# Performance work log

Hardware: AMD Instinct MI355X
Metric: run time of the kernel (lower is better)

Reference implementation:

```python
import jax, jax.numpy as jnp
import numpy as np

MAX_BITS = 64
HIDDEN = 256
EPS = 1e-5
TEMPERATURE = 1.0  # buffer default


def _layernorm(x, gamma, beta):
    mu = jnp.mean(x, axis=-1, keepdims=True)
    var = jnp.var(x, axis=-1, keepdims=True)
    return (x - mu) * jax.lax.rsqrt(var + EPS) * gamma + beta


def setup_inputs() -> dict:
    key = jax.random.key(0)
    ks = jax.random.split(key, 8)
    B = 32768
    # binary-ish inputs in [0,1)
    a_bits = (jax.random.uniform(ks[0], (B, MAX_BITS)) < 0.5).astype(jnp.float32)
    shift_bits = (jax.random.uniform(ks[1], (B, MAX_BITS)) < 0.5).astype(jnp.float32)
    # decoder: Linear(64,256) -> LN -> ReLU -> Linear(256,256) -> LN -> ReLU -> Linear(256,64)
    def lin(k, out_d, in_d):
        bound = 1.0 / np.sqrt(in_d)
        kw, kb = jax.random.split(k)
        W = jax.random.uniform(kw, (out_d, in_d), minval=-bound, maxval=bound)
        b = jax.random.uniform(kb, (out_d,), minval=-bound, maxval=bound)
        return W, b
    W1, b1 = lin(ks[2], HIDDEN, MAX_BITS)
    W2, b2 = lin(ks[3], HIDDEN, HIDDEN)
    W3, b3 = lin(ks[4], MAX_BITS, HIDDEN)
    g1 = jnp.ones((HIDDEN,)); be1 = jnp.zeros((HIDDEN,))
    g2 = jnp.ones((HIDDEN,)); be2 = jnp.zeros((HIDDEN,))
    return {
        "a_bits": a_bits, "shift_bits": shift_bits,
        "W1": W1, "b1": b1, "g1": g1, "be1": be1,
        "W2": W2, "b2": b2, "g2": g2, "be2": be2,
        "W3": W3, "b3": b3,
    }


def reference(a_bits, shift_bits, W1, b1, g1, be1, W2, b2, g2, be2, W3, b3):
    bits = a_bits.shape[1]
    # 2-layer MLP decoder
    h = jax.nn.relu(_layernorm(shift_bits @ W1.T + b1, g1, be1))
    h = jax.nn.relu(_layernorm(h @ W2.T + b2, g2, be2))
    shift_logits = (h @ W3.T + b3)[:, :bits]
    # training path: softmax over shift positions
    shift_probs = jax.nn.softmax(shift_logits / TEMPERATURE, axis=-1)
    # Toeplitz shift-sum: out[b,i] = sum_{s<=i} probs[b,s] * a_bits[b,i-s]
    i = jnp.arange(bits)[:, None]
    s = jnp.arange(bits)[None, :]
    idx = i - s                       # [bits, bits]
    mask = (idx >= 0)
    gath = a_bits[:, jnp.where(mask, idx, 0)] * mask.astype(a_bits.dtype)  # [B, bits, bits]
    return jnp.einsum('bis,bs->bi', gath, shift_probs)
```

## Files before the change

kernel.cpp:

```cpp
#include <hip/hip_runtime.h>
#include <hip/hip_fp16.h>


typedef short s8v __attribute__((ext_vector_type(8)));
typedef float f4v __attribute__((ext_vector_type(4)));

#define HPAD 264
#define PPAD 68

#define OFF_W1F 0
#define OFF_W2F 16384
#define OFF_W3F 81920
#define OFF_B1  98304
#define OFF_G1  98560
#define OFF_BE1 98816
#define OFF_B2  99072
#define OFF_G2  99328
#define OFF_BE2 99584
#define OFF_B3  99840

__device__ __forceinline__ float b2f(unsigned short u) {
    union { unsigned int i; float f; } v; v.i = ((unsigned int)u) << 16; return v.f;
}
__device__ __forceinline__ unsigned short f2b(float f) {
    union { float f; unsigned int i; } v; v.f = f;
    return (unsigned short)((v.i + 0x7fffu + ((v.i >> 16) & 1u)) >> 16);
}
__device__ __forceinline__ unsigned int cvtpk(float a, float b) {
    unsigned int r;
    asm("v_cvt_pk_bf16_f32 %0, %1, %2" : "=v"(r) : "v"(a), "v"(b));
    return r;
}
__device__ __forceinline__ int h2i(__half2 h) { union { __half2 h; int i; } u; u.h = h; return u.i; }
__device__ __forceinline__ __half2 i2h(int i) { union { __half2 h; int i; } u; u.i = i; return u.h; }

__device__ __forceinline__ bool probe_bf16(const void* a_bits) {
    unsigned int wv = ((const unsigned int*)a_bits)[threadIdx.x & 63];
    return __ballot((wv & 0xffffu) == 0x3f80u) != 0ULL;
}

__global__ __launch_bounds__(256) void convert_kernel(
    const void* __restrict__ a_probe,
    const void* __restrict__ W1, const void* __restrict__ W2, const void* __restrict__ W3,
    const void* __restrict__ b1, const void* __restrict__ g1, const void* __restrict__ be1,
    const void* __restrict__ b2, const void* __restrict__ g2, const void* __restrict__ be2,
    const void* __restrict__ b3,
    unsigned short* __restrict__ ws)
{
    const bool isbf = probe_bf16(a_probe);
    const int t = blockIdx.x * 256 + threadIdx.x;

    if (t < 12288) {
        const void* W; int K, idx, dstbase;
        if (t < 2048)       { idx = t;         W = W1; K = 64;  dstbase = OFF_W1F + idx * 8; }
        else if (t < 10240) { idx = t - 2048;  W = W2; K = 256; dstbase = OFF_W2F + idx * 8; }
        else                { idx = t - 10240; W = W3; K = 256; dstbase = OFF_W3F + idx * 8; }
        int nt, kc, lane;
        if (t < 2048) { nt = idx >> 7; kc = (idx >> 6) & 1; lane = idx & 63; }
        else          { nt = idx >> 9; kc = (idx >> 6) & 7; lane = idx & 63; }
        const int row = nt * 16 + (lane & 15);
        const int col = kc * 32 + (lane >> 4) * 8;
        const int src = row * K + col;
        s8v o;
        if (isbf) {
            o = *(const s8v*)((const unsigned short*)W + src);
        } else {
            const float* f = (const float*)W + src;
#pragma unroll
            for (int j = 0; j < 8; ++j) o[j] = (short)f2b(f[j]);
        }
        *(s8v*)(ws + dstbase) = o;
    } else if (t < 12488) {
        const int v = t - 12288;
        const void* srcp; int base, off;
        if (v < 32)       { srcp = b1;  base = OFF_B1;  off = v * 8; }
        else if (v < 64)  { srcp = g1;  base = OFF_G1;  off = (v - 32) * 8; }
        else if (v < 96)  { srcp = be1; base = OFF_BE1; off = (v - 64) * 8; }
        else if (v < 128) { srcp = b2;  base = OFF_B2;  off = (v - 96) * 8; }
        else if (v < 160) { srcp = g2;  base = OFF_G2;  off = (v - 128) * 8; }
        else if (v < 192) { srcp = be2; base = OFF_BE2; off = (v - 160) * 8; }
        else              { srcp = b3;  base = OFF_B3;  off = (v - 192) * 8; }
#pragma unroll
        for (int j = 0; j < 8; ++j)
            ws[base + off + j] = isbf ? ((const unsigned short*)srcp)[off + j]
                                      : f2b(((const float*)srcp)[off + j]);
    }
}

template<bool BF16>
__device__ __forceinline__ float loadS(const void* p, int idx) {
    if constexpr (BF16) return b2f(((const unsigned short*)p)[idx]);
    else return ((const float*)p)[idx];
}
template<bool BF16>
__device__ __forceinline__ s8v loadA8(const void* p, int idx) {
    if constexpr (BF16) {
        return *(const s8v*)((const unsigned short*)p + idx);
    } else {
        const float* f = (const float*)p + idx;
        f4v a = *(const f4v*)f;
        f4v b = *(const f4v*)(f + 4);
        union { s8v s; unsigned int u[4]; } r;
        r.u[0] = cvtpk(a[0], a[1]);
        r.u[1] = cvtpk(a[2], a[3]);
        r.u[2] = cvtpk(b[0], b[1]);
        r.u[3] = cvtpk(b[2], b[3]);
        return r.s;
    }
}
template<bool BF16>
__device__ __forceinline__ void storeO(void* p, int idx, float v) {
    if constexpr (BF16) ((unsigned short*)p)[idx] = f2b(v);
    else ((float*)p)[idx] = v;
}

__device__ __forceinline__ void ln_relu_store(
    f4v* acc, const unsigned short* ws, int offB, int offG, int offBe,
    short* Hs, float* SS, int w, int q, int c, int row, int ntb)
{
    float sm[2][4], sv[2][4];
#pragma unroll
    for (int mt = 0; mt < 2; ++mt)
#pragma unroll
        for (int r = 0; r < 4; ++r) { sm[mt][r] = 0.f; sv[mt][r] = 0.f; }
#pragma unroll
    for (int i = 0; i < 4; ++i) {
        const float bias = b2f(ws[offB + (ntb + i) * 16 + c]);
#pragma unroll
        for (int mt = 0; mt < 2; ++mt)
#pragma unroll
            for (int r = 0; r < 4; ++r) {
                float v = acc[mt * 4 + i][r] + bias;
                acc[mt * 4 + i][r] = v;
                sm[mt][r] += v; sv[mt][r] += v * v;
            }
    }
#pragma unroll
    for (int m = 1; m <= 8; m <<= 1)
#pragma unroll
        for (int mt = 0; mt < 2; ++mt)
#pragma unroll
            for (int r = 0; r < 4; ++r) {
                sm[mt][r] += __shfl_xor(sm[mt][r], m, 64);
                sv[mt][r] += __shfl_xor(sv[mt][r], m, 64);
            }
    if (c == 0)
#pragma unroll
        for (int mt = 0; mt < 2; ++mt)
#pragma unroll
            for (int r = 0; r < 4; ++r) {
                const int g = mt * 16 + row + r;
                *(float2*)&SS[g * 8 + w * 2] = make_float2(sm[mt][r], sv[mt][r]);
            }
    __syncthreads();
#pragma unroll
    for (int mt = 0; mt < 2; ++mt)
#pragma unroll
        for (int r = 0; r < 4; ++r) {
            const int g = mt * 16 + row + r;
            f4v v0 = *(const f4v*)&SS[g * 8];
            f4v v1 = *(const f4v*)&SS[g * 8 + 4];
            float st = v0[0] + v0[2] + v1[0] + v1[2];
            float sq = v0[1] + v0[3] + v1[1] + v1[3];
            float mean = st * (1.0f / 256.0f);
            float var  = fmaxf(sq * (1.0f / 256.0f) - mean * mean, 0.0f);
            sm[mt][r] = mean; sv[mt][r] = rsqrtf(var + 1e-5f);
        }
#pragma unroll
    for (int i = 0; i < 4; ++i) {
        const int nt = ntb + i;
        const float gg = b2f(ws[offG + nt * 16 + c]);
        const float bb = b2f(ws[offBe + nt * 16 + c]);
#pragma unroll
        for (int mt = 0; mt < 2; ++mt) {
            float y[4];
#pragma unroll
            for (int r = 0; r < 4; ++r)
                y[r] = fmaxf((acc[mt * 4 + i][r] - sm[mt][r]) * sv[mt][r] * gg + bb, 0.0f);
            unsigned int u01 = cvtpk(y[0], y[1]);
            unsigned int u23 = cvtpk(y[2], y[3]);
            Hs[(mt * 16 + row + 0) * HPAD + nt * 16 + c] = (short)(u01 & 0xffffu);
            Hs[(mt * 16 + row + 1) * HPAD + nt * 16 + c] = (short)(u01 >> 16);
            Hs[(mt * 16 + row + 2) * HPAD + nt * 16 + c] = (short)(u23 & 0xffffu);
            Hs[(mt * 16 + row + 3) * HPAD + nt * 16 + c] = (short)(u23 >> 16);
        }
    }
}

template<bool BF16>
__device__ __forceinline__ void pipeline(
    const void* a_bits, const void* shifts, const unsigned short* ws, void* out,
    short* Hs, float* Ps, float* SS)
{
    const int tid = threadIdx.x;
    const int w = tid >> 6;
    const int l = tid & 63;
    const int q = l >> 4;
    const int c = l & 15;
    const int ntb = w << 2;
    const int grow0 = (int)blockIdx.x << 5;
    const int row = q * 4;

    f4v acc1[8];
#pragma unroll
    for (int i = 0; i < 8; ++i) acc1[i] = (f4v){0.f, 0.f, 0.f, 0.f};

    const s8v xa00 = loadA8<BF16>(shifts, (grow0 + c) * 64 + q * 8);
    const s8v xa01 = loadA8<BF16>(shifts, (grow0 + c) * 64 + 32 + q * 8);
    const s8v xa10 = loadA8<BF16>(shifts, (grow0 + 16 + c) * 64 + q * 8);
    const s8v xa11 = loadA8<BF16>(shifts, (grow0 + 16 + c) * 64 + 32 + q * 8);
#pragma unroll
    for (int i = 0; i < 4; ++i) {
        const int nt = ntb + i;
        s8v wb0 = *(const s8v*)(ws + OFF_W1F + ((nt * 2 + 0) * 64 + l) * 8);
        s8v wb1 = *(const s8v*)(ws + OFF_W1F + ((nt * 2 + 1) * 64 + l) * 8);
        acc1[i]     = __builtin_amdgcn_mfma_f32_16x16x32_bf16(xa00, wb0, acc1[i], 0, 0, 0);
        acc1[i]     = __builtin_amdgcn_mfma_f32_16x16x32_bf16(xa01, wb1, acc1[i], 0, 0, 0);
        acc1[4 + i] = __builtin_amdgcn_mfma_f32_16x16x32_bf16(xa10, wb0, acc1[4 + i], 0, 0, 0);
        acc1[4 + i] = __builtin_amdgcn_mfma_f32_16x16x32_bf16(xa11, wb1, acc1[4 + i], 0, 0, 0);
    }
    ln_relu_store(acc1, ws, OFF_B1, OFF_G1, OFF_BE1, Hs, SS, w, q, c, row, ntb);
    __syncthreads();

    f4v acc2[8];
#pragma unroll
    for (int i = 0; i < 8; ++i) acc2[i] = (f4v){0.f, 0.f, 0.f, 0.f};
#pragma unroll
    for (int ks = 0; ks < 8; ++ks) {
        s8v af0 = *(const s8v*)&Hs[c * HPAD + ks * 32 + q * 8];
        s8v af1 = *(const s8v*)&Hs[(16 + c) * HPAD + ks * 32 + q * 8];
#pragma unroll
        for (int i = 0; i < 4; ++i) {
            s8v bf_ = *(const s8v*)(ws + OFF_W2F + (((ntb + i) * 8 + ks) * 64 + l) * 8);
            acc2[i]     = __builtin_amdgcn_mfma_f32_16x16x32_bf16(af0, bf_, acc2[i], 0, 0, 0);
            acc2[4 + i] = __builtin_amdgcn_mfma_f32_16x16x32_bf16(af1, bf_, acc2[4 + i], 0, 0, 0);
        }
    }
    ln_relu_store(acc2, ws, OFF_B2, OFF_G2, OFF_BE2, Hs, SS, w, q, c, row, ntb);
    __syncthreads();

    f4v acc3[2];
#pragma unroll
    for (int t = 0; t < 2; ++t) acc3[t] = (f4v){0.f, 0.f, 0.f, 0.f};
#pragma unroll
    for (int ks = 0; ks < 8; ++ks) {
        s8v af0 = *(const s8v*)&Hs[c * HPAD + ks * 32 + q * 8];
        s8v af1 = *(const s8v*)&Hs[(16 + c) * HPAD + ks * 32 + q * 8];
        s8v bf_ = *(const s8v*)(ws + OFF_W3F + ((w * 8 + ks) * 64 + l) * 8);
        acc3[0] = __builtin_amdgcn_mfma_f32_16x16x32_bf16(af0, bf_, acc3[0], 0, 0, 0);
        acc3[1] = __builtin_amdgcn_mfma_f32_16x16x32_bf16(af1, bf_, acc3[1], 0, 0, 0);
    }
    {
        const float bias = b2f(ws[OFF_B3 + w * 16 + c]);
        float sum[2][4];
#pragma unroll
        for (int mt = 0; mt < 2; ++mt)
#pragma unroll
            for (int r = 0; r < 4; ++r) {
                float e = __expf(acc3[mt][r] + bias);
                Ps[(mt * 16 + row + r) * PPAD + w * 16 + c] = e;
                sum[mt][r] = e;
            }
#pragma unroll
        for (int m = 1; m <= 8; m <<= 1)
#pragma unroll
            for (int mt = 0; mt < 2; ++mt)
#pragma unroll
                for (int r = 0; r < 4; ++r)
                    sum[mt][r] += __shfl_xor(sum[mt][r], m, 64);
        if (c == 0)
#pragma unroll
            for (int mt = 0; mt < 2; ++mt)
#pragma unroll
                for (int r = 0; r < 4; ++r)
                    SS[(mt * 16 + row + r) * 8 + w * 2 + 1] = sum[mt][r];
    }
    __syncthreads();

#pragma unroll
    for (int jj = 0; jj < 4; ++jj) {
        const int m0 = w * 8 + jj;
        const int m1 = m0 + 4;
        f4v u0 = *(const f4v*)&SS[m0 * 8];
        f4v u1 = *(const f4v*)&SS[m0 * 8 + 4];
        f4v u2 = *(const f4v*)&SS[m1 * 8];
        f4v u3 = *(const f4v*)&SS[m1 * 8 + 4];
        const float i0 = __builtin_amdgcn_rcpf(u0[1] + u0[3] + u1[1] + u1[3]);
        const float i1 = __builtin_amdgcn_rcpf(u2[1] + u2[3] + u3[1] + u3[3]);
        __half2 pph = __floats2half2_rn(Ps[m0 * PPAD + l] * i0,
                                        Ps[m1 * PPAD + l] * i1);
        const int ppi = h2i(pph);
        __half2 aah = __floats2half2_rn(loadS<BF16>(a_bits, (grow0 + m0) * 64 + l),
                                        loadS<BF16>(a_bits, (grow0 + m1) * 64 + l));
        int rr = h2i(aah);
        __half2 acc = __float2half2_rn(0.0f);
#pragma unroll
        for (int s = 0; s < 64; ++s) {
            const int spi = __builtin_amdgcn_readlane(ppi, s);
            acc = __hfma2(i2h(spi), i2h(rr), acc);
            if (s < 63)
                rr = __builtin_amdgcn_update_dpp(0, rr, 0x138, 0xF, 0xF, true);
        }
        storeO<BF16>(out, (grow0 + m0) * 64 + l, __low2float(acc));
        storeO<BF16>(out, (grow0 + m1) * 64 + l, __high2float(acc));
    }
}

__global__ __launch_bounds__(256, 4) void shiftdec_kernel(
    const void* __restrict__ a_bits, const void* __restrict__ shifts,
    const unsigned short* __restrict__ ws, void* __restrict__ out)
{
    __shared__ __align__(16) short Hs[32 * HPAD];
    __shared__ __align__(16) float Ps[32 * PPAD];
    __shared__ __align__(16) float SSb[32 * 8];

    if (probe_bf16(a_bits))
        pipeline<true>(a_bits, shifts, ws, out, Hs, Ps, SSb);
    else
        pipeline<false>(a_bits, shifts, ws, out, Hs, Ps, SSb);
}

extern "C" void kernel_launch(void* const* d_in, const int* in_sizes, int n_in,
                              void* d_out, int out_size, void* d_ws, size_t ws_size,
                              hipStream_t stream) {
    const int B = in_sizes[0] / 64;
    const int grid = B / 32;

    hipLaunchKernelGGL(convert_kernel, dim3(49), dim3(256), 0, stream,
                       d_in[0], d_in[2], d_in[6], d_in[10],
                       d_in[3], d_in[4], d_in[5], d_in[7], d_in[8], d_in[9], d_in[11],
                       (unsigned short*)d_ws);
    hipLaunchKernelGGL(shiftdec_kernel, dim3(grid), dim3(256), 0, stream,
                       d_in[0], d_in[1], (const unsigned short*)d_ws, d_out);
}
```

Measured before the change: 108.3 us.

## Double rows per block to 64 to reuse weight fragments across more MFMAs

Each block now processes 64 batch rows instead of 32. Every loaded weight fragment (W1, W2, W3) feeds four M-tiles instead of two, which halves global/L2 weight traffic per row and halves the grid size. Accumulator registers and LDS double, and launch bounds drop from 4 to 3 blocks per CU, so occupancy falls and latency hiding may suffer.

```diff
diff --git a/kernel.cpp b/kernel.cpp
--- a/kernel.cpp
+++ b/kernel.cpp
@@ -118,16 +118,16 @@
     f4v* acc, const unsigned short* ws, int offB, int offG, int offBe,
     short* Hs, float* SS, int w, int q, int c, int row, int ntb)
 {
-    float sm[2][4], sv[2][4];
-#pragma unroll
-    for (int mt = 0; mt < 2; ++mt)
+    float sm[4][4], sv[4][4];
+#pragma unroll
+    for (int mt = 0; mt < 4; ++mt)
 #pragma unroll
         for (int r = 0; r < 4; ++r) { sm[mt][r] = 0.f; sv[mt][r] = 0.f; }
 #pragma unroll
     for (int i = 0; i < 4; ++i) {
         const float bias = b2f(ws[offB + (ntb + i) * 16 + c]);
 #pragma unroll
-        for (int mt = 0; mt < 2; ++mt)
+        for (int mt = 0; mt < 4; ++mt)
 #pragma unroll
             for (int r = 0; r < 4; ++r) {
                 float v = acc[mt * 4 + i][r] + bias;
@@ -138,7 +138,7 @@
 #pragma unroll
     for (int m = 1; m <= 8; m <<= 1)
 #pragma unroll
-        for (int mt = 0; mt < 2; ++mt)
+        for (int mt = 0; mt < 4; ++mt)
 #pragma unroll
             for (int r = 0; r < 4; ++r) {
                 sm[mt][r] += __shfl_xor(sm[mt][r], m, 64);
@@ -146,7 +146,7 @@
             }
     if (c == 0)
 #pragma unroll
-        for (int mt = 0; mt < 2; ++mt)
+        for (int mt = 0; mt < 4; ++mt)
 #pragma unroll
             for (int r = 0; r < 4; ++r) {
                 const int g = mt * 16 + row + r;
@@ -154,7 +154,7 @@
             }
     __syncthreads();
 #pragma unroll
-    for (int mt = 0; mt < 2; ++mt)
+    for (int mt = 0; mt < 4; ++mt)
 #pragma unroll
         for (int r = 0; r < 4; ++r) {
             const int g = mt * 16 + row + r;
@@ -172,7 +172,7 @@
         const float gg = b2f(ws[offG + nt * 16 + c]);
         const float bb = b2f(ws[offBe + nt * 16 + c]);
 #pragma unroll
-        for (int mt = 0; mt < 2; ++mt) {
+        for (int mt = 0; mt < 4; ++mt) {
             float y[4];
 #pragma unroll
             for (int r = 0; r < 4; ++r)
@@ -198,63 +198,70 @@
     const int q = l >> 4;
     const int c = l & 15;
     const int ntb = w << 2;
-    const int grow0 = (int)blockIdx.x << 5;
+    const int grow0 = (int)blockIdx.x << 6;
     const int row = q * 4;
 
-    f4v acc1[8];
-#pragma unroll
-    for (int i = 0; i < 8; ++i) acc1[i] = (f4v){0.f, 0.f, 0.f, 0.f};
-
-    const s8v xa00 = loadA8<BF16>(shifts, (grow0 + c) * 64 + q * 8);
-    const s8v xa01 = loadA8<BF16>(shifts, (grow0 + c) * 64 + 32 + q * 8);
-    const s8v xa10 = loadA8<BF16>(shifts, (grow0 + 16 + c) * 64 + q * 8);
-    const s8v xa11 = loadA8<BF16>(shifts, (grow0 + 16 + c) * 64 + 32 + q * 8);
+    f4v acc1[16];
+#pragma unroll
+    for (int i = 0; i < 16; ++i) acc1[i] = (f4v){0.f, 0.f, 0.f, 0.f};
+
+    s8v xa[4][2];
+#pragma unroll
+    for (int mt = 0; mt < 4; ++mt) {
+        xa[mt][0] = loadA8<BF16>(shifts, (grow0 + mt * 16 + c) * 64 + q * 8);
+        xa[mt][1] = loadA8<BF16>(shifts, (grow0 + mt * 16 + c) * 64 + 32 + q * 8);
+    }
 #pragma unroll
     for (int i = 0; i < 4; ++i) {
         const int nt = ntb + i;
         s8v wb0 = *(const s8v*)(ws + OFF_W1F + ((nt * 2 + 0) * 64 + l) * 8);
         s8v wb1 = *(const s8v*)(ws + OFF_W1F + ((nt * 2 + 1) * 64 + l) * 8);
-        acc1[i]     = __builtin_amdgcn_mfma_f32_16x16x32_bf16(xa00, wb0, acc1[i], 0, 0, 0);
-        acc1[i]     = __builtin_amdgcn_mfma_f32_16x16x32_bf16(xa01, wb1, acc1[i], 0, 0, 0);
-        acc1[4 + i] = __builtin_amdgcn_mfma_f32_16x16x32_bf16(xa10, wb0, acc1[4 + i], 0, 0, 0);
-        acc1[4 + i] = __builtin_amdgcn_mfma_f32_16x16x32_bf16(xa11, wb1, acc1[4 + i], 0, 0, 0);
+#pragma unroll
+        for (int mt = 0; mt < 4; ++mt) {
+            acc1[mt * 4 + i] = __builtin_amdgcn_mfma_f32_16x16x32_bf16(xa[mt][0], wb0, acc1[mt * 4 + i], 0, 0, 0);
+            acc1[mt * 4 + i] = __builtin_amdgcn_mfma_f32_16x16x32_bf16(xa[mt][1], wb1, acc1[mt * 4 + i], 0, 0, 0);
+        }
     }
     ln_relu_store(acc1, ws, OFF_B1, OFF_G1, OFF_BE1, Hs, SS, w, q, c, row, ntb);
     __syncthreads();
 
-    f4v acc2[8];
-#pragma unroll
-    for (int i = 0; i < 8; ++i) acc2[i] = (f4v){0.f, 0.f, 0.f, 0.f};
+    f4v acc2[16];
+#pragma unroll
+    for (int i = 0; i < 16; ++i) acc2[i] = (f4v){0.f, 0.f, 0.f, 0.f};
 #pragma unroll
     for (int ks = 0; ks < 8; ++ks) {
-        s8v af0 = *(const s8v*)&Hs[c * HPAD + ks * 32 + q * 8];
-        s8v af1 = *(const s8v*)&Hs[(16 + c) * HPAD + ks * 32 + q * 8];
+        s8v af[4];
+#pragma unroll
+        for (int mt = 0; mt < 4; ++mt)
+            af[mt] = *(const s8v*)&Hs[(mt * 16 + c) * HPAD + ks * 32 + q * 8];
 #pragma unroll
         for (int i = 0; i < 4; ++i) {
             s8v bf_ = *(const s8v*)(ws + OFF_W2F + (((ntb + i) * 8 + ks) * 64 + l) * 8);
-            acc2[i]     = __builtin_amdgcn_mfma_f32_16x16x32_bf16(af0, bf_, acc2[i], 0, 0, 0);
-            acc2[4 + i] = __builtin_amdgcn_mfma_f32_16x16x32_bf16(af1, bf_, acc2[4 + i], 0, 0, 0);
+#pragma unroll
+            for (int mt = 0; mt < 4; ++mt)
+                acc2[mt * 4 + i] = __builtin_amdgcn_mfma_f32_16x16x32_bf16(af[mt], bf_, acc2[mt * 4 + i], 0, 0, 0);
         }
     }
     ln_relu_store(acc2, ws, OFF_B2, OFF_G2, OFF_BE2, Hs, SS, w, q, c, row, ntb);
     __syncthreads();
 
-    f4v acc3[2];
-#pragma unroll
-    for (int t = 0; t < 2; ++t) acc3[t] = (f4v){0.f, 0.f, 0.f, 0.f};
+    f4v acc3[4];
+#pragma unroll
+    for (int t = 0; t < 4; ++t) acc3[t] = (f4v){0.f, 0.f, 0.f, 0.f};
 #pragma unroll
     for (int ks = 0; ks < 8; ++ks) {
-        s8v af0 = *(const s8v*)&Hs[c * HPAD + ks * 32 + q * 8];
-        s8v af1 = *(const s8v*)&Hs[(16 + c) * HPAD + ks * 32 + q * 8];
         s8v bf_ = *(const s8v*)(ws + OFF_W3F + ((w * 8 + ks) * 64 + l) * 8);
-        acc3[0] = __builtin_amdgcn_mfma_f32_16x16x32_bf16(af0, bf_, acc3[0], 0, 0, 0);
-        acc3[1] = __builtin_amdgcn_mfma_f32_16x16x32_bf16(af1, bf_, acc3[1], 0, 0, 0);
+#pragma unroll
+        for (int mt = 0; mt < 4; ++mt) {
+            s8v af = *(const s8v*)&Hs[(mt * 16 + c) * HPAD + ks * 32 + q * 8];
+            acc3[mt] = __builtin_amdgcn_mfma_f32_16x16x32_bf16(af, bf_, acc3[mt], 0, 0, 0);
+        }
     }
     {
         const float bias = b2f(ws[OFF_B3 + w * 16 + c]);
-        float sum[2][4];
-#pragma unroll
-        for (int mt = 0; mt < 2; ++mt)
+        float sum[4][4];
+#pragma unroll
+        for (int mt = 0; mt < 4; ++mt)
 #pragma unroll
             for (int r = 0; r < 4; ++r) {
                 float e = __expf(acc3[mt][r] + bias);
@@ -264,13 +271,13 @@
 #pragma unroll
         for (int m = 1; m <= 8; m <<= 1)
 #pragma unroll
-            for (int mt = 0; mt < 2; ++mt)
+            for (int mt = 0; mt < 4; ++mt)
 #pragma unroll
                 for (int r = 0; r < 4; ++r)
                     sum[mt][r] += __shfl_xor(sum[mt][r], m, 64);
         if (c == 0)
 #pragma unroll
-            for (int mt = 0; mt < 2; ++mt)
+            for (int mt = 0; mt < 4; ++mt)
 #pragma unroll
                 for (int r = 0; r < 4; ++r)
                     SS[(mt * 16 + row + r) * 8 + w * 2 + 1] = sum[mt][r];
@@ -278,9 +285,9 @@
     __syncthreads();
 
 #pragma unroll
-    for (int jj = 0; jj < 4; ++jj) {
-        const int m0 = w * 8 + jj;
-        const int m1 = m0 + 4;
+    for (int jj = 0; jj < 8; ++jj) {
+        const int m0 = w * 16 + jj;
+        const int m1 = m0 + 8;
         f4v u0 = *(const f4v*)&SS[m0 * 8];
         f4v u1 = *(const f4v*)&SS[m0 * 8 + 4];
         f4v u2 = *(const f4v*)&SS[m1 * 8];
@@ -306,13 +313,13 @@
     }
 }
 
-__global__ __launch_bounds__(256, 4) void shiftdec_kernel(
+__global__ __launch_bounds__(256, 3) void shiftdec_kernel(
     const void* __restrict__ a_bits, const void* __restrict__ shifts,
     const unsigned short* __restrict__ ws, void* __restrict__ out)
 {
-    __shared__ __align__(16) short Hs[32 * HPAD];
-    __shared__ __align__(16) float Ps[32 * PPAD];
-    __shared__ __align__(16) float SSb[32 * 8];
+    __shared__ __align__(16) short Hs[64 * HPAD];
+    __shared__ __align__(16) float Ps[64 * PPAD];
+    __shared__ __align__(16) float SSb[64 * 8];
 
     if (probe_bf16(a_bits))
         pipeline<true>(a_bits, shifts, ws, out, Hs, Ps, SSb);
@@ -324,7 +331,7 @@
                               void* d_out, int out_size, void* d_ws, size_t ws_size,
                               hipStream_t stream) {
     const int B = in_sizes[0] / 64;
-    const int grid = B / 32;
+    const int grid = B / 64;
 
     hipLaunchKernelGGL(convert_kernel, dim3(49), dim3(256), 0, stream,
                        d_in[0], d_in[2], d_in[6], d_in[10],
```

New measurement: 123.2 us. +13.7%, slower.
